# Kernel optimization log

Hardware: AMD Instinct MI355X
Metric: run time of the kernel (lower is better)

## Reference

```python
import jax, jax.numpy as jnp
import numpy as np

B, S, H, R, NH = 4, 2048, 1024, 512, 8
HD = R // NH
EPS = 1e-5


def _ln(x, g, b):
    m = jnp.mean(x, axis=-1, keepdims=True)
    v = jnp.mean(jnp.square(x - m), axis=-1, keepdims=True)
    return (x - m) * jax.lax.rsqrt(v + EPS) * g + b


def setup_inputs() -> dict:
    key = jax.random.key(0)
    ks = iter(jax.random.split(key, 40))
    s = 0.02
    d = {}
    d['hidden_states'] = jax.random.normal(next(ks), (B, S, H), dtype=jnp.float32)
    # complexity assessor: H -> H//4 -> 32 -> 1
    d['ca_w1'] = jax.random.normal(next(ks), (H, H // 4)) * s
    d['ca_b1'] = jnp.zeros((H // 4,))
    d['ca_w2'] = jax.random.normal(next(ks), (H // 4, 32)) * s
    d['ca_b2'] = jnp.zeros((32,))
    d['ca_w3'] = jax.random.normal(next(ks), (32, 1)) * s
    d['ca_b3'] = jnp.zeros((1,))
    # reasoning projection H -> R, and pre-norm
    d['rp_w'] = jax.random.normal(next(ks), (H, R)) * s
    d['rp_b'] = jnp.zeros((R,))
    d['rn_g'] = jnp.ones((R,)); d['rn_b'] = jnp.zeros((R,))
    # transformer encoder layer (norm_first)
    d['ln1_g'] = jnp.ones((R,)); d['ln1_b'] = jnp.zeros((R,))
    d['wqkv'] = jax.random.normal(next(ks), (R, 3 * R)) * s
    d['bqkv'] = jnp.zeros((3 * R,))
    d['wo'] = jax.random.normal(next(ks), (R, R)) * s
    d['bo'] = jnp.zeros((R,))
    d['ln2_g'] = jnp.ones((R,)); d['ln2_b'] = jnp.zeros((R,))
    d['ff1_w'] = jax.random.normal(next(ks), (R, 4 * R)) * s
    d['ff1_b'] = jnp.zeros((4 * R,))
    d['ff2_w'] = jax.random.normal(next(ks), (4 * R, R)) * s
    d['ff2_b'] = jnp.zeros((R,))
    # output projection R -> H and norm
    d['op_w'] = jax.random.normal(next(ks), (R, H)) * s
    d['op_b'] = jnp.zeros((H,))
    d['on_g'] = jnp.ones((H,)); d['on_b'] = jnp.zeros((H,))
    # integration gate: 2H -> H -> H
    d['gw1'] = jax.random.normal(next(ks), (2 * H, H)) * s
    d['gb1'] = jnp.zeros((H,))
    d['gw2'] = jax.random.normal(next(ks), (H, H)) * s
    d['gb2'] = jnp.zeros((H,))
    return d


def reference(hidden_states, ca_w1, ca_b1, ca_w2, ca_b2, ca_w3, ca_b3,
              rp_w, rp_b, rn_g, rn_b, ln1_g, ln1_b, wqkv, bqkv, wo, bo,
              ln2_g, ln2_b, ff1_w, ff1_b, ff2_w, ff2_b, op_w, op_b,
              on_g, on_b, gw1, gb1, gw2, gb2):
    # complexity assessment (metrics only; input_ids=None forces reasoning on all)
    pooled = jnp.mean(hidden_states, axis=1)  # [B,H]
    h = jax.nn.relu(pooled @ ca_w1 + ca_b1)
    h = jax.nn.relu(h @ ca_w2 + ca_b2)
    complexity_scores = jax.nn.sigmoid(h @ ca_w3 + ca_b3)[:, 0]  # [B]

    # apply_reasoning on full batch (should_reason is all-True)
    r = _ln(hidden_states @ rp_w + rp_b, rn_g, rn_b)  # [B,S,R]

    # TransformerEncoderLayer, norm_first, relu, dropout=0
    y = _ln(r, ln1_g, ln1_b)
    qkv = y @ wqkv + bqkv
    q, k, v = jnp.split(qkv, 3, axis=-1)
    q = q.reshape(B, S, NH, HD)
    k = k.reshape(B, S, NH, HD)
    v = v.reshape(B, S, NH, HD)
    scores = jnp.einsum('bqhd,bkhd->bhqk', q, k) / np.sqrt(HD).astype(np.float32)
    attn = jax.nn.softmax(scores, axis=-1)
    o = jnp.einsum('bhqk,bkhd->bqhd', attn, v).reshape(B, S, R)
    r = r + (o @ wo + bo)
    y = _ln(r, ln2_g, ln2_b)
    r = r + (jax.nn.relu(y @ ff1_w + ff1_b) @ ff2_w + ff2_b)

    reasoned = _ln(r @ op_w + op_b, on_g, on_b)  # [B,S,H]

    # sigmoid integration gate on concat([states, reasoned])
    gate_in = jnp.concatenate([hidden_states, reasoned], axis=-1)
    g = jax.nn.relu(gate_in @ gw1 + gb1)
    g = jax.nn.sigmoid(g @ gw2 + gb2)
    output = hidden_states + g * reasoned
    return output, complexity_scores
```

## Files before the change

kernel.cpp:

```cpp
#include <hip/hip_runtime.h>
#include <hip/hip_bf16.h>
#include <math.h>


typedef __bf16 bf16;
typedef __attribute__((ext_vector_type(8))) __bf16 bf16x8;
typedef __attribute__((ext_vector_type(4))) float f32x4;

__device__ __forceinline__ void glds16(const bf16* g, bf16* l) {
  __builtin_amdgcn_global_load_lds(
      (const __attribute__((address_space(1))) void*)g,
      (__attribute__((address_space(3))) void*)l, 16, 0, 0);
}

__global__ void k_transpose_cvt(const float* __restrict__ in, bf16* __restrict__ out,
                                int rows, int cols) {
  __shared__ float tile[32][33];
  int c0 = blockIdx.x * 32, r0 = blockIdx.y * 32;
  int tx = threadIdx.x, ty = threadIdx.y;
  for (int i = 0; i < 32; i += 8)
    tile[ty + i][tx] = in[(long)(r0 + ty + i) * cols + (c0 + tx)];
  __syncthreads();
  for (int i = 0; i < 32; i += 8)
    out[(long)(c0 + ty + i) * rows + (r0 + tx)] = (bf16)tile[tx][ty + i];
}

__global__ void k_transpose_f32(const float* __restrict__ in, float* __restrict__ out,
                                int rows, int cols) {
  __shared__ float tile[32][33];
  int c0 = blockIdx.x * 32, r0 = blockIdx.y * 32;
  int tx = threadIdx.x, ty = threadIdx.y;
  for (int i = 0; i < 32; i += 8)
    tile[ty + i][tx] = in[(long)(r0 + ty + i) * cols + (c0 + tx)];
  __syncthreads();
  for (int i = 0; i < 32; i += 8)
    out[(long)(c0 + ty + i) * rows + (r0 + tx)] = tile[tx][ty + i];
}

__global__ void k_cvt(const float* __restrict__ in, bf16* __restrict__ out) {
  long i = ((long)blockIdx.x * 256 + threadIdx.x) * 4;
  float4 v = *(const float4*)(in + i);
  bf16* o = out + i;
  o[0] = (bf16)v.x; o[1] = (bf16)v.y; o[2] = (bf16)v.z; o[3] = (bf16)v.w;
}

__global__ void k_vtrans(const bf16* __restrict__ qkv, bf16* __restrict__ VT) {
  __shared__ bf16 tile[32][33];
  int bh = blockIdx.z, b = bh >> 3, h = bh & 7;
  const bf16* in = qkv + (long)b * 2048 * 1536 + 1024 + h * 64;
  bf16* out = VT + (long)bh * 64 * 2048;
  int c0 = blockIdx.x * 32, r0 = blockIdx.y * 32;
  int tx = threadIdx.x, ty = threadIdx.y;
  for (int i = 0; i < 32; i += 8)
    tile[ty + i][tx] = in[(long)(r0 + ty + i) * 1536 + (c0 + tx)];
  __syncthreads();
  for (int i = 0; i < 32; i += 8)
    out[(long)(c0 + ty + i) * 2048 + (r0 + tx)] = tile[tx][ty + i];
}

__global__ void k_pool_part(const float* __restrict__ X, float* __restrict__ part) {
  int b = blockIdx.y, c = blockIdx.z;
  int col = blockIdx.x * 256 + threadIdx.x;
  const float* p = X + (long)b * 2048 * 1024 + (long)c * 128 * 1024 + col;
  float s = 0.f;
  for (int i = 0; i < 128; i++) s += p[(long)i * 1024];
  part[((long)c * 4 + b) * 1024 + col] = s;
}

__global__ void k_pool_fin(const float* __restrict__ part, float* __restrict__ pooled) {
  int idx = blockIdx.x * 256 + threadIdx.x;
  int b = idx >> 10, col = idx & 1023;
  float s = 0.f;
  for (int c = 0; c < 16; c++) s += part[((long)c * 4 + b) * 1024 + col];
  pooled[idx] = s * (1.0f / 2048.0f);
}

__global__ void k_ca1(const float* __restrict__ pooled, const float* __restrict__ w1T,
                      const float* __restrict__ b1, float* __restrict__ h1) {
  int t = blockIdx.x, b = threadIdx.x >> 6, lane = threadIdx.x & 63;
  const float* wr = w1T + (long)t * 1024 + lane * 16;
  const float* pr = pooled + b * 1024 + lane * 16;
  float acc = 0.f;
  for (int j = 0; j < 4; j++) {
    float4 w = *(const float4*)(wr + j * 4);
    float4 p = *(const float4*)(pr + j * 4);
    acc += w.x * p.x + w.y * p.y + w.z * p.z + w.w * p.w;
  }
  for (int off = 32; off; off >>= 1) acc += __shfl_xor(acc, off);
  if (lane == 0) h1[b * 256 + t] = fmaxf(acc + b1[t], 0.f);
}

__global__ void k_ca2(const float* __restrict__ h1,
                      const float* __restrict__ w2, const float* __restrict__ b2,
                      const float* __restrict__ w3, const float* __restrict__ b3,
                      float* __restrict__ scores) {
  __shared__ float w2s[256 * 32];
  __shared__ float h1s[4 * 256];
  __shared__ float h2s[4][32];
  int t = threadIdx.x;
  for (int j = 0; j < 32; j++) w2s[j * 256 + t] = w2[j * 256 + t];
  for (int j = 0; j < 4; j++) h1s[j * 256 + t] = h1[j * 256 + t];
  __syncthreads();
  if (t < 128) {
    int b = t >> 5, o = t & 31;
    float acc = b2[o];
    for (int k = 0; k < 256; k++) acc += h1s[b * 256 + k] * w2s[k * 32 + o];
    h2s[b][o] = fmaxf(acc, 0.f);
  }
  __syncthreads();
  if (t < 4) {
    float acc = b3[0];
    for (int k = 0; k < 32; k++) acc += h2s[t][k] * w3[k];
    scores[t] = 1.f / (1.f + expf(-acc));
  }
}

template <int NCOL>
__global__ void k_ln(const bf16* __restrict__ in, const float* __restrict__ g,
                     const float* __restrict__ be, bf16* __restrict__ out) {
  int wave = threadIdx.x >> 6, lane = threadIdx.x & 63;
  long row = (long)blockIdx.x * 4 + wave;
  const bf16* x = in + row * NCOL;
  constexpr int PER = NCOL / 64;
  constexpr int CH = PER / 8;
  float v[PER];
  float s = 0.f;
  for (int c = 0; c < CH; c++) {
    bf16x8 t = *(const bf16x8*)(x + c * 512 + lane * 8);
    for (int j = 0; j < 8; j++) { v[c * 8 + j] = (float)t[j]; s += v[c * 8 + j]; }
  }
  for (int off = 32; off; off >>= 1) s += __shfl_xor(s, off);
  float mean = s * (1.0f / NCOL);
  float q = 0.f;
  for (int i = 0; i < PER; i++) { float d = v[i] - mean; q += d * d; }
  for (int off = 32; off; off >>= 1) q += __shfl_xor(q, off);
  float rstd = rsqrtf(q * (1.0f / NCOL) + 1e-5f);
  for (int c = 0; c < CH; c++) {
    bf16x8 o;
    for (int j = 0; j < 8; j++) {
      int col = c * 512 + lane * 8 + j;
      o[j] = (bf16)((v[c * 8 + j] - mean) * rstd * g[col] + be[col]);
    }
    *(bf16x8*)(out + row * NCOL + c * 512 + lane * 8) = o;
  }
}

__global__ void k_ln2(const bf16* __restrict__ in,
                      const float* __restrict__ g1, const float* __restrict__ b1,
                      const float* __restrict__ g2, const float* __restrict__ b2,
                      bf16* __restrict__ outR, bf16* __restrict__ outY) {
  int wave = threadIdx.x >> 6, lane = threadIdx.x & 63;
  long row = (long)blockIdx.x * 4 + wave;
  const bf16* x = in + row * 512;
  float v[8];
  float s = 0.f;
  bf16x8 t = *(const bf16x8*)(x + lane * 8);
  for (int j = 0; j < 8; j++) { v[j] = (float)t[j]; s += v[j]; }
  for (int off = 32; off; off >>= 1) s += __shfl_xor(s, off);
  float mean = s * (1.0f / 512);
  float q = 0.f;
  for (int j = 0; j < 8; j++) { float d = v[j] - mean; q += d * d; }
  for (int off = 32; off; off >>= 1) q += __shfl_xor(q, off);
  float rstd = rsqrtf(q * (1.0f / 512) + 1e-5f);
  float r[8];
  float s2 = 0.f;
  bf16x8 orr;
  for (int j = 0; j < 8; j++) {
    int col = lane * 8 + j;
    r[j] = (v[j] - mean) * rstd * g1[col] + b1[col];
    orr[j] = (bf16)r[j];
    s2 += r[j];
  }
  *(bf16x8*)(outR + row * 512 + lane * 8) = orr;
  for (int off = 32; off; off >>= 1) s2 += __shfl_xor(s2, off);
  float mean2 = s2 * (1.0f / 512);
  float q2 = 0.f;
  for (int j = 0; j < 8; j++) { float d = r[j] - mean2; q2 += d * d; }
  for (int off = 32; off; off >>= 1) q2 += __shfl_xor(q2, off);
  float rstd2 = rsqrtf(q2 * (1.0f / 512) + 1e-5f);
  bf16x8 oy;
  for (int j = 0; j < 8; j++) {
    int col = lane * 8 + j;
    oy[j] = (bf16)((r[j] - mean2) * rstd2 * g2[col] + b2[col]);
  }
  *(bf16x8*)(outY + row * 512 + lane * 8) = oy;
}

template <int EPI, int MT>
__launch_bounds__(256, 2)
__global__ void k_gemm(const bf16* __restrict__ A1, int ldA1,
                       const bf16* __restrict__ B1, int ldB1, int K1,
                       const bf16* __restrict__ A2, int ldA2,
                       const bf16* __restrict__ B2, int ldB2, int K2,
                       const float* __restrict__ bias, void* __restrict__ out,
                       int ldOut, const bf16* __restrict__ resid, int ldRes,
                       const float* __restrict__ auxX, const bf16* __restrict__ auxR) {
  __shared__ __align__(16) bf16 As[MT * 32];
  __shared__ __align__(16) bf16 Bs[128 * 32];
  constexpr int NF = (MT == 128) ? 4 : 2;
  constexpr int NW = (MT == 128) ? 64 : 32;
  int t = threadIdx.x;
  int wave = t >> 6, lane = t & 63, quad = lane >> 4, l16 = lane & 15;
  int wy = (MT == 128) ? (wave >> 1) : 0;
  int wx = (MT == 128) ? (wave & 1) : wave;
  int m0 = blockIdx.y * MT, n0 = blockIdx.x * 128;
  int sr = t >> 2;
  int sc = (t & 3) * 8;
  bf16* la0 = As + wave * 512;
  bf16* la1 = As + 2048 + wave * 512;
  bf16* lb0 = Bs + wave * 512;
  bf16* lb1 = Bs + 2048 + wave * 512;

  f32x4 acc[4][NF] = {};

  auto run = [&](const bf16* A, int ldA, const bf16* Bt, int ldB, int K) {
    const bf16* ag0 = A + (long)(m0 + sr) * ldA + sc;
    const bf16* ag1 = ag0 + (long)64 * ldA;
    const bf16* bg0 = Bt + (long)(n0 + sr) * ldB + sc;
    const bf16* bg1 = bg0 + (long)64 * ldB;
    for (int kt = 0; kt < K; kt += 32) {
      glds16(ag0 + kt, la0);
      if constexpr (MT == 128) glds16(ag1 + kt, la1);
      glds16(bg0 + kt, lb0);
      glds16(bg1 + kt, lb1);
      __syncthreads();
      bf16x8 af[4], bfr[NF];
      for (int im = 0; im < 4; im++)
        af[im] = *(const bf16x8*)(As + (64 * wy + 16 * im + l16) * 32 + quad * 8);
      for (int in = 0; in < NF; in++)
        bfr[in] = *(const bf16x8*)(Bs + (NW * wx + 16 * in + l16) * 32 + quad * 8);
      for (int im = 0; im < 4; im++)
        for (int in = 0; in < NF; in++)
          acc[im][in] = __builtin_amdgcn_mfma_f32_16x16x32_bf16(af[im], bfr[in],
                                                                acc[im][in], 0, 0, 0);
      __syncthreads();
    }
  };
  run(A1, ldA1, B1, ldB1, K1);
  if (A2) run(A2, ldA2, B2, ldB2, K2);

  int rb = m0 + 64 * wy + quad * 4;
  int cb = n0 + NW * wx + l16;
  for (int im = 0; im < 4; im++)
    for (int in = 0; in < NF; in++)
      for (int i = 0; i < 4; i++) {
        int row = rb + 16 * im + i;
        int col = cb + 16 * in;
        long o = (long)row * ldOut + col;
        float v = acc[im][in][i] + bias[col];
        if constexpr (EPI == 0) ((bf16*)out)[o] = (bf16)v;
        else if constexpr (EPI == 1) ((bf16*)out)[o] = (bf16)fmaxf(v, 0.f);
        else if constexpr (EPI == 2)
          ((bf16*)out)[o] = (bf16)(v + (float)resid[(long)row * ldRes + col]);
        else {
          float gg = 1.f / (1.f + expf(-v));
          ((float*)out)[o] = auxX[o] + gg * (float)auxR[o];
        }
      }
}

__launch_bounds__(256, 4)
__global__ void k_attn(const bf16* __restrict__ qkv, const bf16* __restrict__ VT,
                       bf16* __restrict__ o_out) {
  __shared__ __align__(16) bf16 Qs[64 * 72];
  __shared__ __align__(16) bf16 Ks[64 * 72];
  __shared__ __align__(16) bf16 Vs[64 * 72];
  __shared__ __align__(16) bf16 Ps[64 * 72];
  int t = threadIdx.x, wave = t >> 6, lane = t & 63, quad = lane >> 4, l16 = lane & 15;
  int q0 = blockIdx.x * 64;
  int h = blockIdx.y, b = blockIdx.z;
  const bf16* qb = qkv + (long)b * 2048 * 1536 + h * 64;
  const bf16* vb = VT + (long)(b * 8 + h) * 64 * 2048;

  for (int i = 0; i < 2; i++) {
    int idx = i * 256 + t, q = idx >> 3, cg = idx & 7;
    *(uint4*)(Qs + q * 72 + cg * 8) =
        *(const uint4*)(qb + (long)(q0 + q) * 1536 + cg * 8);
  }
  __syncthreads();
  bf16x8 a0 = *(const bf16x8*)(Qs + (16 * wave + l16) * 72 + quad * 8);
  bf16x8 a1 = *(const bf16x8*)(Qs + (16 * wave + l16) * 72 + 32 + quad * 8);

  float rs[4] = {0.f, 0.f, 0.f, 0.f};
  f32x4 oacc[4] = {};
  const float scale = 0.125f;

  for (int kt = 0; kt < 32; kt++) {
    int k0 = kt * 64;
    __syncthreads();
    for (int i = 0; i < 2; i++) {
      int idx = i * 256 + t, r = idx >> 3, cg = idx & 7;
      *(uint4*)(Ks + r * 72 + cg * 8) =
          *(const uint4*)(qb + 512 + (long)(k0 + r) * 1536 + cg * 8);
      *(uint4*)(Vs + r * 72 + cg * 8) =
          *(const uint4*)(vb + (long)r * 2048 + k0 + cg * 8);
    }
    __syncthreads();

    f32x4 sf[4];
    for (int in = 0; in < 4; in++) {
      bf16x8 b0 = *(const bf16x8*)(Ks + (16 * in + l16) * 72 + quad * 8);
      bf16x8 b1 = *(const bf16x8*)(Ks + (16 * in + l16) * 72 + 32 + quad * 8);
      f32x4 c = {0.f, 0.f, 0.f, 0.f};
      c = __builtin_amdgcn_mfma_f32_16x16x32_bf16(a0, b0, c, 0, 0, 0);
      c = __builtin_amdgcn_mfma_f32_16x16x32_bf16(a1, b1, c, 0, 0, 0);
      sf[in] = c;
    }
    for (int in = 0; in < 4; in++)
      for (int i = 0; i < 4; i++) {
        float p = __expf(sf[in][i] * scale);
        rs[i] += p;
        Ps[(16 * wave + quad * 4 + i) * 72 + 16 * in + l16] = (bf16)p;
      }

    const bf16* pw = Ps + (16 * wave + l16) * 72;
    for (int ks = 0; ks < 2; ks++) {
      bf16x8 ap = *(const bf16x8*)(pw + ks * 32 + quad * 8);
      for (int j = 0; j < 4; j++) {
        bf16x8 bv = *(const bf16x8*)(Vs + (16 * j + l16) * 72 + ks * 32 + quad * 8);
        oacc[j] = __builtin_amdgcn_mfma_f32_16x16x32_bf16(ap, bv, oacc[j], 0, 0, 0);
      }
    }
  }
  for (int i = 0; i < 4; i++)
    for (int off = 1; off < 16; off <<= 1) rs[i] += __shfl_xor(rs[i], off);
  for (int i = 0; i < 4; i++) {
    float inv = 1.f / rs[i];
    int row = q0 + 16 * wave + quad * 4 + i;
    long gr = ((long)b * 2048 + row) * 512 + h * 64;
    for (int j = 0; j < 4; j++)
      o_out[gr + 16 * j + l16] = (bf16)(oacc[j][i] * inv);
  }
}

extern "C" void kernel_launch(void* const* d_in, const int* in_sizes, int n_in,
                              void* d_out, int out_size, void* d_ws, size_t ws_size,
                              hipStream_t stream) {
  const float* X    = (const float*)d_in[0];
  const float* caw1 = (const float*)d_in[1];
  const float* cab1 = (const float*)d_in[2];
  const float* caw2 = (const float*)d_in[3];
  const float* cab2 = (const float*)d_in[4];
  const float* caw3 = (const float*)d_in[5];
  const float* cab3 = (const float*)d_in[6];
  const float* rp_w = (const float*)d_in[7];
  const float* rp_b = (const float*)d_in[8];
  const float* rn_g = (const float*)d_in[9];
  const float* rn_b = (const float*)d_in[10];
  const float* ln1g = (const float*)d_in[11];
  const float* ln1b = (const float*)d_in[12];
  const float* wqkv = (const float*)d_in[13];
  const float* bqkv = (const float*)d_in[14];
  const float* wo   = (const float*)d_in[15];
  const float* bo   = (const float*)d_in[16];
  const float* ln2g = (const float*)d_in[17];
  const float* ln2b = (const float*)d_in[18];
  const float* ff1w = (const float*)d_in[19];
  const float* ff1b = (const float*)d_in[20];
  const float* ff2w = (const float*)d_in[21];
  const float* ff2b = (const float*)d_in[22];
  const float* opw  = (const float*)d_in[23];
  const float* opb  = (const float*)d_in[24];
  const float* ong  = (const float*)d_in[25];
  const float* onb  = (const float*)d_in[26];
  const float* gw1  = (const float*)d_in[27];
  const float* gb1  = (const float*)d_in[28];
  const float* gw2  = (const float*)d_in[29];
  const float* gb2  = (const float*)d_in[30];

  char* ws = (char*)d_ws;
  const size_t MB = 1u << 20;
  const size_t KB = 1u << 10;
  bf16* rpwT  = (bf16*)ws;
  bf16* wqkvT = rpwT + 524288;
  bf16* woT   = wqkvT + 786432;
  bf16* ff1T  = woT + 262144;
  bf16* ff2T  = ff1T + 1048576;
  bf16* opT   = ff2T + 1048576;
  bf16* gw1T  = opT + 524288;
  bf16* gw2T  = gw1T + 2097152;
  float* part   = (float*)(ws + 14 * MB);
  float* pooled = (float*)(ws + 14 * MB + 256 * KB);
  float* h1buf  = (float*)(ws + 14 * MB + 272 * KB);
  bf16* Xb   = (bf16*)(ws + 15 * MB);
  bf16* bufA = (bf16*)(ws + 31 * MB);
  bf16* bufB = (bf16*)(ws + 39 * MB);
  bf16* bufC = (bf16*)(ws + 47 * MB);
  bf16* qkv  = (bf16*)(ws + 55 * MB);
  float* w1T = (float*)(ws + 55 * MB);
  bf16* VT   = (bf16*)(ws + 79 * MB);
  bf16* f1   = (bf16*)(ws + 55 * MB);
  bf16* tmp3 = (bf16*)(ws + 55 * MB);
  bf16* rsn  = (bf16*)(ws + 71 * MB);
  bf16* g1   = (bf16*)(ws + 31 * MB);

  dim3 b32x8(32, 8);
  k_transpose_cvt<<<dim3(16, 32), b32x8, 0, stream>>>(rp_w, rpwT, 1024, 512);
  k_transpose_cvt<<<dim3(48, 16), b32x8, 0, stream>>>(wqkv, wqkvT, 512, 1536);
  k_transpose_cvt<<<dim3(16, 16), b32x8, 0, stream>>>(wo, woT, 512, 512);
  k_transpose_cvt<<<dim3(64, 16), b32x8, 0, stream>>>(ff1w, ff1T, 512, 2048);
  k_transpose_cvt<<<dim3(16, 64), b32x8, 0, stream>>>(ff2w, ff2T, 2048, 512);
  k_transpose_cvt<<<dim3(32, 16), b32x8, 0, stream>>>(opw, opT, 512, 1024);
  k_transpose_cvt<<<dim3(32, 64), b32x8, 0, stream>>>(gw1, gw1T, 2048, 1024);
  k_transpose_cvt<<<dim3(32, 32), b32x8, 0, stream>>>(gw2, gw2T, 1024, 1024);
  k_transpose_f32<<<dim3(8, 32), b32x8, 0, stream>>>(caw1, w1T, 1024, 256);
  k_cvt<<<8192, 256, 0, stream>>>(X, Xb);

  k_pool_part<<<dim3(4, 4, 16), 256, 0, stream>>>(X, part);
  k_pool_fin<<<16, 256, 0, stream>>>(part, pooled);
  k_ca1<<<256, 256, 0, stream>>>(pooled, w1T, cab1, h1buf);
  k_ca2<<<1, 256, 0, stream>>>(h1buf, caw2, cab2, caw3, cab3,
                               (float*)d_out + 8388608);

  k_gemm<0, 64><<<dim3(4, 128), 256, 0, stream>>>(
      Xb, 1024, rpwT, 1024, 1024, nullptr, 0, nullptr, 0, 0,
      rp_b, bufA, 512, nullptr, 0, nullptr, nullptr);
  k_ln2<<<2048, 256, 0, stream>>>(bufA, rn_g, rn_b, ln1g, ln1b, bufB, bufC);
  k_gemm<0, 128><<<dim3(12, 64), 256, 0, stream>>>(
      bufC, 512, wqkvT, 512, 512, nullptr, 0, nullptr, 0, 0,
      bqkv, qkv, 1536, nullptr, 0, nullptr, nullptr);
  k_vtrans<<<dim3(2, 64, 32), b32x8, 0, stream>>>(qkv, VT);
  k_attn<<<dim3(32, 8, 4), 256, 0, stream>>>(qkv, VT, bufC);
  k_gemm<2, 64><<<dim3(4, 128), 256, 0, stream>>>(
      bufC, 512, woT, 512, 512, nullptr, 0, nullptr, 0, 0,
      bo, bufA, 512, bufB, 512, nullptr, nullptr);
  k_ln<512><<<2048, 256, 0, stream>>>(bufA, ln2g, ln2b, bufB);
  k_gemm<1, 128><<<dim3(16, 64), 256, 0, stream>>>(
      bufB, 512, ff1T, 512, 512, nullptr, 0, nullptr, 0, 0,
      ff1b, f1, 2048, nullptr, 0, nullptr, nullptr);
  k_gemm<2, 64><<<dim3(4, 128), 256, 0, stream>>>(
      f1, 2048, ff2T, 2048, 2048, nullptr, 0, nullptr, 0, 0,
      ff2b, bufC, 512, bufA, 512, nullptr, nullptr);
  k_gemm<0, 128><<<dim3(8, 64), 256, 0, stream>>>(
      bufC, 512, opT, 512, 512, nullptr, 0, nullptr, 0, 0,
      opb, tmp3, 1024, nullptr, 0, nullptr, nullptr);
  k_ln<1024><<<2048, 256, 0, stream>>>(tmp3, ong, onb, rsn);
  k_gemm<1, 128><<<dim3(8, 64), 256, 0, stream>>>(
      Xb, 1024, gw1T, 2048, 1024, rsn, 1024, gw1T + 1024, 2048, 1024,
      gb1, g1, 1024, nullptr, 0, nullptr, nullptr);
  k_gemm<5, 128><<<dim3(8, 64), 256, 0, stream>>>(
      g1, 1024, gw2T, 1024, 1024, nullptr, 0, nullptr, 0, 0,
      gb2, (float*)d_out, 1024, nullptr, 0, X, rsn);
}
```

Before: 523.1 us.

## Use 32x32 MFMA with 128-row Q tiles in attention; batch weight transposes

The attention kernel now gives each wave 32 query rows and uses the 32x32x16 bf16 MFMA instead of 16x16x32. Each K/V tile loaded into shared memory is therefore reused across twice as many queries, and the grid halves. The Q buffer is reused as the P staging buffer, and launch bounds drop to 2 blocks per SM because more registers are needed. Separately, the nine weight-transpose launches are merged into one kernel driven by a descriptor table, cutting launch overhead. The risks are lower occupancy and fewer blocks (512) to cover the GPU.

```diff
diff --git a/kernel.cpp b/kernel.cpp
--- a/kernel.cpp
+++ b/kernel.cpp
@@ -6,6 +6,7 @@
 typedef __bf16 bf16;
 typedef __attribute__((ext_vector_type(8))) __bf16 bf16x8;
 typedef __attribute__((ext_vector_type(4))) float f32x4;
+typedef __attribute__((ext_vector_type(16))) float f32x16;
 
 __device__ __forceinline__ void glds16(const bf16* g, bf16* l) {
   __builtin_amdgcn_global_load_lds(
@@ -13,28 +14,31 @@
       (__attribute__((address_space(3))) void*)l, 16, 0, 0);
 }
 
-__global__ void k_transpose_cvt(const float* __restrict__ in, bf16* __restrict__ out,
-                                int rows, int cols) {
+struct TD { const float* src; char* dst; int rows, cols, tx, start, outbf; };
+struct TDs { TD d[9]; };
+__global__ void k_trans_all(TDs td) {
+  int bid = blockIdx.x;
+  int si = 0;
+  for (int i = 1; i < 9; i++)
+    if (bid >= td.d[i].start) si = i;
+  TD dd = td.d[si];
+  int tid = bid - dd.start;
+  int bx = tid % dd.tx, by = tid / dd.tx;
   __shared__ float tile[32][33];
-  int c0 = blockIdx.x * 32, r0 = blockIdx.y * 32;
+  int c0 = bx * 32, r0 = by * 32;
   int tx = threadIdx.x, ty = threadIdx.y;
   for (int i = 0; i < 32; i += 8)
-    tile[ty + i][tx] = in[(long)(r0 + ty + i) * cols + (c0 + tx)];
+    tile[ty + i][tx] = dd.src[(long)(r0 + ty + i) * dd.cols + (c0 + tx)];
   __syncthreads();
-  for (int i = 0; i < 32; i += 8)
-    out[(long)(c0 + ty + i) * rows + (r0 + tx)] = (bf16)tile[tx][ty + i];
-}
-
-__global__ void k_transpose_f32(const float* __restrict__ in, float* __restrict__ out,
-                                int rows, int cols) {
-  __shared__ float tile[32][33];
-  int c0 = blockIdx.x * 32, r0 = blockIdx.y * 32;
-  int tx = threadIdx.x, ty = threadIdx.y;
-  for (int i = 0; i < 32; i += 8)
-    tile[ty + i][tx] = in[(long)(r0 + ty + i) * cols + (c0 + tx)];
-  __syncthreads();
-  for (int i = 0; i < 32; i += 8)
-    out[(long)(c0 + ty + i) * rows + (r0 + tx)] = tile[tx][ty + i];
+  if (dd.outbf) {
+    bf16* o = (bf16*)dd.dst;
+    for (int i = 0; i < 32; i += 8)
+      o[(long)(c0 + ty + i) * dd.rows + (r0 + tx)] = (bf16)tile[tx][ty + i];
+  } else {
+    float* o = (float*)dd.dst;
+    for (int i = 0; i < 32; i += 8)
+      o[(long)(c0 + ty + i) * dd.rows + (r0 + tx)] = tile[tx][ty + i];
+  }
 }
 
 __global__ void k_cvt(const float* __restrict__ in, bf16* __restrict__ out) {
@@ -259,30 +263,32 @@
       }
 }
 
-__launch_bounds__(256, 4)
+__launch_bounds__(256, 2)
 __global__ void k_attn(const bf16* __restrict__ qkv, const bf16* __restrict__ VT,
                        bf16* __restrict__ o_out) {
-  __shared__ __align__(16) bf16 Qs[64 * 72];
   __shared__ __align__(16) bf16 Ks[64 * 72];
   __shared__ __align__(16) bf16 Vs[64 * 72];
-  __shared__ __align__(16) bf16 Ps[64 * 72];
-  int t = threadIdx.x, wave = t >> 6, lane = t & 63, quad = lane >> 4, l16 = lane & 15;
-  int q0 = blockIdx.x * 64;
+  __shared__ __align__(16) bf16 PQs[128 * 72];
+  int t = threadIdx.x, wave = t >> 6, lane = t & 63;
+  int l32 = lane & 31, half = lane >> 5;
+  int q0 = blockIdx.x * 128;
   int h = blockIdx.y, b = blockIdx.z;
   const bf16* qb = qkv + (long)b * 2048 * 1536 + h * 64;
   const bf16* vb = VT + (long)(b * 8 + h) * 64 * 2048;
 
-  for (int i = 0; i < 2; i++) {
+  for (int i = 0; i < 4; i++) {
     int idx = i * 256 + t, q = idx >> 3, cg = idx & 7;
-    *(uint4*)(Qs + q * 72 + cg * 8) =
+    *(uint4*)(PQs + q * 72 + cg * 8) =
         *(const uint4*)(qb + (long)(q0 + q) * 1536 + cg * 8);
   }
   __syncthreads();
-  bf16x8 a0 = *(const bf16x8*)(Qs + (16 * wave + l16) * 72 + quad * 8);
-  bf16x8 a1 = *(const bf16x8*)(Qs + (16 * wave + l16) * 72 + 32 + quad * 8);
-
-  float rs[4] = {0.f, 0.f, 0.f, 0.f};
-  f32x4 oacc[4] = {};
+  bf16x8 qf[4];
+  for (int c = 0; c < 4; c++)
+    qf[c] = *(const bf16x8*)(PQs + (wave * 32 + l32) * 72 + c * 16 + half * 8);
+
+  float rs[16];
+  for (int i = 0; i < 16; i++) rs[i] = 0.f;
+  f32x16 oacc[2] = {};
   const float scale = 0.125f;
 
   for (int kt = 0; kt < 32; kt++) {
@@ -297,39 +303,35 @@
     }
     __syncthreads();
 
-    f32x4 sf[4];
-    for (int in = 0; in < 4; in++) {
-      bf16x8 b0 = *(const bf16x8*)(Ks + (16 * in + l16) * 72 + quad * 8);
-      bf16x8 b1 = *(const bf16x8*)(Ks + (16 * in + l16) * 72 + 32 + quad * 8);
-      f32x4 c = {0.f, 0.f, 0.f, 0.f};
-      c = __builtin_amdgcn_mfma_f32_16x16x32_bf16(a0, b0, c, 0, 0, 0);
-      c = __builtin_amdgcn_mfma_f32_16x16x32_bf16(a1, b1, c, 0, 0, 0);
-      sf[in] = c;
-    }
-    for (int in = 0; in < 4; in++)
-      for (int i = 0; i < 4; i++) {
-        float p = __expf(sf[in][i] * scale);
-        rs[i] += p;
-        Ps[(16 * wave + quad * 4 + i) * 72 + 16 * in + l16] = (bf16)p;
+    for (int kb = 0; kb < 2; kb++) {
+      f32x16 s = {};
+      for (int c = 0; c < 4; c++) {
+        bf16x8 kf = *(const bf16x8*)(Ks + (kb * 32 + l32) * 72 + c * 16 + half * 8);
+        s = __builtin_amdgcn_mfma_f32_32x32x16_bf16(qf[c], kf, s, 0, 0, 0);
       }
-
-    const bf16* pw = Ps + (16 * wave + l16) * 72;
-    for (int ks = 0; ks < 2; ks++) {
-      bf16x8 ap = *(const bf16x8*)(pw + ks * 32 + quad * 8);
-      for (int j = 0; j < 4; j++) {
-        bf16x8 bv = *(const bf16x8*)(Vs + (16 * j + l16) * 72 + ks * 32 + quad * 8);
-        oacc[j] = __builtin_amdgcn_mfma_f32_16x16x32_bf16(ap, bv, oacc[j], 0, 0, 0);
+      for (int r = 0; r < 16; r++) {
+        float p = __expf(s[r] * scale);
+        rs[r] += p;
+        int row = (r & 3) + 8 * (r >> 2) + 4 * half;
+        PQs[(wave * 32 + row) * 72 + kb * 32 + l32] = (bf16)p;
       }
     }
-  }
-  for (int i = 0; i < 4; i++)
-    for (int off = 1; off < 16; off <<= 1) rs[i] += __shfl_xor(rs[i], off);
-  for (int i = 0; i < 4; i++) {
-    float inv = 1.f / rs[i];
-    int row = q0 + 16 * wave + quad * 4 + i;
+    for (int c = 0; c < 4; c++) {
+      bf16x8 pf = *(const bf16x8*)(PQs + (wave * 32 + l32) * 72 + c * 16 + half * 8);
+      for (int db = 0; db < 2; db++) {
+        bf16x8 vf = *(const bf16x8*)(Vs + (db * 32 + l32) * 72 + c * 16 + half * 8);
+        oacc[db] = __builtin_amdgcn_mfma_f32_32x32x16_bf16(pf, vf, oacc[db], 0, 0, 0);
+      }
+    }
+  }
+  for (int r = 0; r < 16; r++)
+    for (int off = 1; off < 32; off <<= 1) rs[r] += __shfl_xor(rs[r], off);
+  for (int r = 0; r < 16; r++) {
+    float inv = 1.f / rs[r];
+    int row = q0 + wave * 32 + (r & 3) + 8 * (r >> 2) + 4 * half;
     long gr = ((long)b * 2048 + row) * 512 + h * 64;
-    for (int j = 0; j < 4; j++)
-      o_out[gr + 16 * j + l16] = (bf16)(oacc[j][i] * inv);
+    o_out[gr + l32] = (bf16)(oacc[0][r] * inv);
+    o_out[gr + 32 + l32] = (bf16)(oacc[1][r] * inv);
   }
 }
 
@@ -394,16 +396,18 @@
   bf16* rsn  = (bf16*)(ws + 71 * MB);
   bf16* g1   = (bf16*)(ws + 31 * MB);
 
+  TDs td;
+  td.d[0] = {rp_w, (char*)rpwT, 1024, 512, 16, 0, 1};
+  td.d[1] = {wqkv, (char*)wqkvT, 512, 1536, 48, 512, 1};
+  td.d[2] = {wo, (char*)woT, 512, 512, 16, 1280, 1};
+  td.d[3] = {ff1w, (char*)ff1T, 512, 2048, 64, 1536, 1};
+  td.d[4] = {ff2w, (char*)ff2T, 2048, 512, 16, 2560, 1};
+  td.d[5] = {opw, (char*)opT, 512, 1024, 32, 3584, 1};
+  td.d[6] = {gw1, (char*)gw1T, 2048, 1024, 32, 4096, 1};
+  td.d[7] = {gw2, (char*)gw2T, 1024, 1024, 32, 6144, 1};
+  td.d[8] = {caw1, (char*)w1T, 1024, 256, 8, 7168, 0};
   dim3 b32x8(32, 8);
-  k_transpose_cvt<<<dim3(16, 32), b32x8, 0, stream>>>(rp_w, rpwT, 1024, 512);
-  k_transpose_cvt<<<dim3(48, 16), b32x8, 0, stream>>>(wqkv, wqkvT, 512, 1536);
-  k_transpose_cvt<<<dim3(16, 16), b32x8, 0, stream>>>(wo, woT, 512, 512);
-  k_transpose_cvt<<<dim3(64, 16), b32x8, 0, stream>>>(ff1w, ff1T, 512, 2048);
-  k_transpose_cvt<<<dim3(16, 64), b32x8, 0, stream>>>(ff2w, ff2T, 2048, 512);
-  k_transpose_cvt<<<dim3(32, 16), b32x8, 0, stream>>>(opw, opT, 512, 1024);
-  k_transpose_cvt<<<dim3(32, 64), b32x8, 0, stream>>>(gw1, gw1T, 2048, 1024);
-  k_transpose_cvt<<<dim3(32, 32), b32x8, 0, stream>>>(gw2, gw2T, 1024, 1024);
-  k_transpose_f32<<<dim3(8, 32), b32x8, 0, stream>>>(caw1, w1T, 1024, 256);
+  k_trans_all<<<7424, b32x8, 0, stream>>>(td);
   k_cvt<<<8192, 256, 0, stream>>>(X, Xb);
 
   k_pool_part<<<dim3(4, 4, 16), 256, 0, stream>>>(X, part);
@@ -420,7 +424,7 @@
       bufC, 512, wqkvT, 512, 512, nullptr, 0, nullptr, 0, 0,
       bqkv, qkv, 1536, nullptr, 0, nullptr, nullptr);
   k_vtrans<<<dim3(2, 64, 32), b32x8, 0, stream>>>(qkv, VT);
-  k_attn<<<dim3(32, 8, 4), 256, 0, stream>>>(qkv, VT, bufC);
+  k_attn<<<dim3(16, 8, 4), 256, 0, stream>>>(qkv, VT, bufC);
   k_gemm<2, 64><<<dim3(4, 128), 256, 0, stream>>>(
       bufC, 512, woT, 512, 512, nullptr, 0, nullptr, 0, 0,
       bo, bufA, 512, bufB, 512, nullptr, nullptr);
```

After: 511.2 us. 2.3% less time.
